# Performance work log

Hardware: AMD Instinct MI355X
Metric: run time of the kernel (lower is better)

Reference implementation:

```python
import jax, jax.numpy as jnp
import numpy as np

B, S, H = 2, 1024, 2048
NH, NKV, HD = 32, 8, 64
EPS = 1e-6
ROPE_BASE = 10000.0


def rms_norm(x, w, eps=EPS):
    xf = x.astype(jnp.float32)
    var = jnp.mean(xf * xf, axis=-1, keepdims=True)
    return (w * (xf * jax.lax.rsqrt(var + eps))).astype(x.dtype)


def rotate_half(x):
    x1, x2 = jnp.split(x, 2, axis=-1)
    return jnp.concatenate((-x2, x1), axis=-1)


def setup_inputs() -> dict:
    key = jax.random.key(0)
    ks = jax.random.split(key, 8)
    hidden_states = jax.random.normal(ks[0], (B, S, H), dtype=jnp.float32) * 0.02
    # real rotary embeddings for positions 0..S-1
    inv_freq = 1.0 / (ROPE_BASE ** (jnp.arange(0, HD, 2, dtype=jnp.float32) / HD))
    freqs = jnp.arange(S, dtype=jnp.float32)[:, None] * inv_freq[None, :]  # [S, HD/2]
    emb = jnp.concatenate((freqs, freqs), axis=-1)  # [S, HD]
    cos = jnp.broadcast_to(jnp.cos(emb)[None], (B, S, HD)).astype(jnp.float32)
    sin = jnp.broadcast_to(jnp.sin(emb)[None], (B, S, HD)).astype(jnp.float32)
    # additive causal mask [B, 1, S, S]
    causal = jnp.tril(jnp.ones((S, S), dtype=bool))
    attention_mask = jnp.broadcast_to(
        jnp.where(causal, 0.0, -1e9).astype(jnp.float32)[None, None], (B, 1, S, S))
    scale_in = 1.0 / np.sqrt(H)
    wq = jax.random.normal(ks[1], (H, NH * HD), dtype=jnp.float32) * scale_in
    wk = jax.random.normal(ks[2], (H, NKV * HD), dtype=jnp.float32) * scale_in
    wv = jax.random.normal(ks[3], (H, NKV * HD), dtype=jnp.float32) * scale_in
    wo = jax.random.normal(ks[4], (NH * HD, H), dtype=jnp.float32) * scale_in
    q_norm_w = jnp.ones((NH * HD,), dtype=jnp.float32)
    k_norm_w = jnp.ones((NKV * HD,), dtype=jnp.float32)
    return {"hidden_states": hidden_states, "cos": cos, "sin": sin,
            "attention_mask": attention_mask, "wq": wq, "wk": wk, "wv": wv,
            "wo": wo, "q_norm_w": q_norm_w, "k_norm_w": k_norm_w}


def reference(hidden_states, cos, sin, attention_mask, wq, wk, wv, wo, q_norm_w, k_norm_w):
    b, s, _ = hidden_states.shape
    scaling = HD ** -0.5
    groups = NH // NKV
    # projections + QK-norm (RMSNorm over full projected dim, before head split)
    q = rms_norm(hidden_states @ wq, q_norm_w)
    k = rms_norm(hidden_states @ wk, k_norm_w)
    v = hidden_states @ wv
    q = q.reshape(b, s, NH, HD).transpose(0, 2, 1, 3)   # [b, nh, s, hd]
    k = k.reshape(b, s, NKV, HD).transpose(0, 2, 1, 3)  # [b, nkv, s, hd]
    v = v.reshape(b, s, NKV, HD).transpose(0, 2, 1, 3)
    # RoPE (cos/sin broadcast over head dim)
    c = cos[:, None]  # [b, 1, s, hd]
    sn = sin[:, None]
    q = q * c + rotate_half(q) * sn
    k = k * c + rotate_half(k) * sn
    # GQA: repeat KV heads
    k = jnp.repeat(k, groups, axis=1)  # [b, nh, s, hd]
    v = jnp.repeat(v, groups, axis=1)
    scores = jnp.einsum('bhqd,bhkd->bhqk', q, k) * scaling + attention_mask
    attn = jax.nn.softmax(scores.astype(jnp.float32), axis=-1).astype(q.dtype)
    out = jnp.einsum('bhqk,bhkd->bhqd', attn, v)
    out = out.transpose(0, 2, 1, 3).reshape(b, s, NH * HD)
    return out @ wo
```

## Files before the change

kernel.cpp:

```cpp
#include <hip/hip_runtime.h>

#define B_    2
#define S_    1024
#define NH_   32
#define NKV_  8
#define T_    (B_*S_)

typedef unsigned short u16;
typedef unsigned int u32;
typedef __attribute__((ext_vector_type(8))) short bf16x8;
typedef __attribute__((ext_vector_type(4))) float f32x4;

__device__ __forceinline__ float bf2f(u16 u) {
    union { float f; unsigned int i; } c; c.i = ((unsigned int)u) << 16; return c.f;
}
__device__ __forceinline__ u32 cvtpk(float lo, float hi) {
    u32 r;
    asm("v_cvt_pk_bf16_f32 %0, %1, %2" : "=v"(r) : "v"(lo), "v"(hi));
    return r;
}
__device__ __forceinline__ u16 f2bf(float f) {
    return (u16)cvtpk(f, 0.f);
}

__device__ __forceinline__ void gld_lds16(const void* g, void* s) {
    __builtin_amdgcn_global_load_lds(
        (const __attribute__((address_space(1))) void*)g,
        (__attribute__((address_space(3))) void*)s,
        16, 0, 0);
}

__global__ __launch_bounds__(256) void preproc1(
    const float* __restrict__ hidden, const float* __restrict__ wq,
    const float* __restrict__ wk, const float* __restrict__ wv,
    const float* __restrict__ wo,
    u16* __restrict__ hidden_bf, u16* __restrict__ wqkvT, u16* __restrict__ woT)
{
    __shared__ float t[64][65];
    const int bid = blockIdx.x, tid = threadIdx.x;
    if (bid < 2048) {
        int i = (bid * 256 + tid) * 8;
        float4 v0 = *reinterpret_cast<const float4*>(&hidden[i]);
        float4 v1 = *reinterpret_cast<const float4*>(&hidden[i + 4]);
        u32 ow[4] = { cvtpk(v0.x, v0.y), cvtpk(v0.z, v0.w),
                      cvtpk(v1.x, v1.y), cvtpk(v1.z, v1.w) };
        *reinterpret_cast<uint4*>(&hidden_bf[i]) = *reinterpret_cast<uint4*>(ow);
        return;
    }
    const float* src; int scol, sN, n0, k0;
    u16* dst; int dK;
    if (bid < 3584) {
        const int tt = bid - 2048;
        n0 = (tt % 48) * 64; k0 = (tt / 48) * 64;
        if (n0 < 2048)      { src = wq; scol = n0;        sN = 2048; }
        else if (n0 < 2560) { src = wk; scol = n0 - 2048; sN = 512;  }
        else                { src = wv; scol = n0 - 2560; sN = 512;  }
        dst = wqkvT; dK = 2048;
    } else {
        const int tt = bid - 3584;
        n0 = (tt % 32) * 64; k0 = (tt / 32) * 64;
        src = wo; scol = n0; sN = 2048;
        dst = woT; dK = 2048;
    }
    #pragma unroll
    for (int i = 0; i < 4; ++i) {
        int e = i * 256 + tid, r = e >> 4, c4 = (e & 15) * 4;
        float4 v = *reinterpret_cast<const float4*>(
            &src[(size_t)(k0 + r) * sN + scol + c4]);
        t[r][c4 + 0] = v.x;
        t[r][c4 + 1] = v.y;
        t[r][c4 + 2] = v.z;
        t[r][c4 + 3] = v.w;
    }
    __syncthreads();
    #pragma unroll
    for (int i = 0; i < 4; ++i) {
        int e = i * 256 + tid, rr = e >> 4, cc4 = (e & 15) * 4;
        u32 ow[2] = { cvtpk(t[cc4][rr], t[cc4 + 1][rr]),
                      cvtpk(t[cc4 + 2][rr], t[cc4 + 3][rr]) };
        *reinterpret_cast<uint2*>(&dst[(size_t)(n0 + rr) * dK + k0 + cc4])
            = *reinterpret_cast<uint2*>(ow);
    }
}

template<int BM, int BN, bool OUT_BF16>
__global__ __launch_bounds__(256) void gemm_bt(
    const u16* __restrict__ A, const u16* __restrict__ Bt,
    void* __restrict__ Cv, int M, int N, int K)
{
    constexpr int FM  = BM / 32;
    constexpr int FN  = BN / 32;
    constexpr int ACH = BM / 32;
    constexpr int BCH = BN / 32;
    __shared__ u16 As[2][BM * 64];
    __shared__ u16 Bs[2][BN * 64];
    const int MB = M / BM;
    const int mpx = MB >> 3;
    const int xcd = blockIdx.x & 7, lid = blockIdx.x >> 3;
    const int bm = (xcd * mpx + (lid % mpx)) * BM;
    const int bn = (lid / mpx) * BN;
    const int tid = threadIdx.x;
    const int w = tid >> 6, lane = tid & 63;
    const int wr = w >> 1, wc = w & 1;
    const int l15 = lane & 15, lg = lane >> 4;
    const int srow = lane >> 3;
    const int scolsw = (lane & 7) ^ srow;

    f32x4 acc[FM][FN] = {};
    const int nk = K >> 6;

#define GSTAGE(ks, bb) do {                                                    \
    const int kofs = (ks) * 64;                                                \
    _Pragma("unroll")                                                          \
    for (int i_ = 0; i_ < ACH; ++i_) {                                         \
        int chunk_ = w * ACH + i_;                                             \
        int row_ = chunk_ * 8 + srow;                                          \
        gld_lds16(&A[(size_t)(bm + row_) * K + kofs + scolsw * 8],             \
                  &As[bb][chunk_ * 512]);                                      \
    }                                                                          \
    _Pragma("unroll")                                                          \
    for (int j_ = 0; j_ < BCH; ++j_) {                                         \
        int chunk_ = w * BCH + j_;                                             \
        int row_ = chunk_ * 8 + srow;                                          \
        gld_lds16(&Bt[(size_t)(bn + row_) * K + kofs + scolsw * 8],            \
                  &Bs[bb][chunk_ * 512]);                                      \
    } } while (0)

    GSTAGE(0, 0);
    for (int ks = 0; ks < nk; ++ks) {
        const int cur = ks & 1;
        if (ks + 1 < nk) {
            GSTAGE(ks + 1, cur ^ 1);
            if (ACH + BCH == 6)      { asm volatile("s_waitcnt vmcnt(6)" ::: "memory"); }
            else if (ACH + BCH == 4) { asm volatile("s_waitcnt vmcnt(4)" ::: "memory"); }
            else                     { asm volatile("s_waitcnt vmcnt(0)" ::: "memory"); }
        } else {
            asm volatile("s_waitcnt vmcnt(0)" ::: "memory");
        }
        __builtin_amdgcn_s_barrier();
        __builtin_amdgcn_sched_barrier(0);

        #pragma unroll
        for (int kk = 0; kk < 2; ++kk) {
            const int phys = ((kk * 4 + lg) ^ (l15 & 7)) * 8;
            bf16x8 a[FM], b[FN];
            #pragma unroll
            for (int m = 0; m < FM; ++m)
                a[m] = *reinterpret_cast<const bf16x8*>(
                    &As[cur][(wr * (BM / 2) + m * 16 + l15) * 64 + phys]);
            #pragma unroll
            for (int n = 0; n < FN; ++n)
                b[n] = *reinterpret_cast<const bf16x8*>(
                    &Bs[cur][(wc * (BN / 2) + n * 16 + l15) * 64 + phys]);
            #pragma unroll
            for (int m = 0; m < FM; ++m)
                #pragma unroll
                for (int n = 0; n < FN; ++n)
                    acc[m][n] = __builtin_amdgcn_mfma_f32_16x16x32_bf16(
                        a[m], b[n], acc[m][n], 0, 0, 0);
        }
        __builtin_amdgcn_s_barrier();
    }
#undef GSTAGE

    const int orow0 = bm + wr * (BM / 2), ocol0 = bn + wc * (BN / 2);
    #pragma unroll
    for (int m = 0; m < FM; ++m)
        #pragma unroll
        for (int n = 0; n < FN; ++n)
            #pragma unroll
            for (int r = 0; r < 4; ++r) {
                int row = orow0 + m * 16 + lg * 4 + r;
                int col = ocol0 + n * 16 + l15;
                float v = acc[m][n][r];
                if (OUT_BF16)
                    ((u16*)Cv)[(size_t)row * N + col] = f2bf(v);
                else
                    ((float*)Cv)[(size_t)row * N + col] = v;
            }
}

template<int DIM>
__device__ __forceinline__ void rms_rope_row(
    u16* base, const float* __restrict__ w,
    const float* __restrict__ cs, const float* __restrict__ sn,
    float* row, float* red, int tid, float osc)
{
    float ss = 0.f;
    for (int i0 = tid * 8; i0 < DIM; i0 += 2048) {
        uint4 u = *reinterpret_cast<const uint4*>(&base[i0]);
        const u16* us = reinterpret_cast<const u16*>(&u);
        #pragma unroll
        for (int j = 0; j < 8; ++j) { float f = bf2f(us[j]); row[i0 + j] = f; ss += f * f; }
    }
    #pragma unroll
    for (int off = 1; off < 64; off <<= 1) ss += __shfl_xor(ss, off);
    if ((tid & 63) == 0) red[tid >> 6] = ss;
    __syncthreads();
    const float rstd = rsqrtf((red[0] + red[1] + red[2] + red[3]) * (1.0f / DIM) + 1e-6f);

    for (int i0 = tid * 8; i0 < DIM; i0 += 2048) {
        float ov[8];
        #pragma unroll
        for (int j = 0; j < 8; ++j) {
            int i = i0 + j, dh = i & 63, bb = i & ~63;
            int oi = (dh < 32) ? bb + dh + 32 : bb + dh - 32;
            float y     = row[i]  * rstd * w[i];
            float other = row[oi] * rstd * w[oi];
            if (dh < 32) other = -other;
            ov[j] = (y * cs[dh] + other * sn[dh]) * osc;
        }
        u32 ow[4] = { cvtpk(ov[0], ov[1]), cvtpk(ov[2], ov[3]),
                      cvtpk(ov[4], ov[5]), cvtpk(ov[6], ov[7]) };
        *reinterpret_cast<uint4*>(&base[i0]) = *reinterpret_cast<uint4*>(ow);
    }
}

__global__ __launch_bounds__(256) void rmsnorm_rope_vt(
    u16* __restrict__ x, const float* __restrict__ qnw, const float* __restrict__ knw,
    const float* __restrict__ cosb, const float* __restrict__ sinb,
    u16* __restrict__ vT)
{
    __shared__ float smem[2304];
    const int bid = blockIdx.x, tid = threadIdx.x;
    if (bid < 2048) {
        const int t = bid;
        float* row = smem;
        float* red = smem + 2048;
        const float* cs = cosb + (size_t)t * 64;
        const float* sn = sinb + (size_t)t * 64;
        rms_rope_row<2048>(x + (size_t)t * 3072,        qnw, cs, sn, row, red, tid,
                           0.18033688f);
        __syncthreads();
        rms_rope_row<512 >(x + (size_t)t * 3072 + 2048, knw, cs, sn, row, red, tid,
                           1.0f);
        return;
    }
    u16 (*tu)[72] = reinterpret_cast<u16(*)[72]>(smem);
    const int bid2 = bid - 2048;
    const int hd = bid2 % 16;
    const int s0 = (bid2 / 16) * 64;
    const int b = hd >> 3, kvh = hd & 7;
    #pragma unroll
    for (int i = 0; i < 2; ++i) {
        int chunk = i * 256 + tid;
        int r = chunk >> 3, c8 = (chunk & 7) * 8;
        uint4 u = *reinterpret_cast<const uint4*>(
            &x[(size_t)(b * 1024 + s0 + r) * 3072 + 2560 + kvh * 64 + c8]);
        *reinterpret_cast<uint4*>(&tu[r][c8]) = u;
    }
    __syncthreads();
    #pragma unroll
    for (int i = 0; i < 2; ++i) {
        int chunk = i * 256 + tid;
        int d = chunk >> 3, c8 = (chunk & 7) * 8;
        u16 o[8];
        #pragma unroll
        for (int j = 0; j < 8; ++j) o[j] = tu[c8 + j][d];
        *reinterpret_cast<uint4*>(&vT[((size_t)(hd * 64 + d)) * 1024 + s0 + c8])
            = *reinterpret_cast<uint4*>(o);
    }
}

__global__ __launch_bounds__(256) void attn_tb(
    const u16* __restrict__ qkv,
    const u16* __restrict__ vT,
    u16* __restrict__ ob)
{
    __shared__ u16 Ks[3][64 * 64];
    __shared__ u16 Vs[3][64 * 64];
    __shared__ u16 Ps[4][16 * 64];

    const int bid = blockIdx.x;
    const int L   = (bid & 7) * 64 + (bid >> 3);
    const int g5  = L >> 5;
    const int rem = L & 31;
    const int ha  = rem & 3;
    const int p   = rem >> 2;
    const int b = g5 >> 3, kvh = g5 & 7;
    const int h = kvh * 4 + ha;
    const int qtA = p, qtB = 15 - p;

    const int tid = threadIdx.x, w = tid >> 6, lane = tid & 63;
    const int l15 = lane & 15, lg = lane >> 4;
    const int srow = lane >> 3;
    const int scolsw = (lane & 7) ^ srow;

    bf16x8 qfA[2], qfB[2];
    {
        const size_t rA = (size_t)(b * 1024 + qtA * 64 + w * 16 + l15);
        const size_t rB = (size_t)(b * 1024 + qtB * 64 + w * 16 + l15);
        #pragma unroll
        for (int kk = 0; kk < 2; ++kk) {
            qfA[kk] = *reinterpret_cast<const bf16x8*>(
                &qkv[rA * 3072 + h * 64 + kk * 32 + lg * 8]);
            qfB[kk] = *reinterpret_cast<const bf16x8*>(
                &qkv[rB * 3072 + h * 64 + kk * 32 + lg * 8]);
        }
    }
    asm volatile("s_waitcnt vmcnt(0)" ::: "memory");

    float lrA = 0.f, lrB = 0.f;
    f32x4 oaccA[4] = {}, oaccB[4] = {};

    const u16* kbase = qkv + 2048 + kvh * 64;
    const u16* vbase = vT + (size_t)(g5 * 64) * 1024;
    const int qgA = qtA * 64 + w * 16 + l15;
    const int qgB = qtB * 64 + w * 16 + l15;

#define ASTAGE(kt, bb) do {                                                    \
    _Pragma("unroll")                                                          \
    for (int i_ = 0; i_ < 2; ++i_) {                                           \
        int chunk_ = w * 2 + i_;                                               \
        int row_ = chunk_ * 8 + srow;                                          \
        gld_lds16(&kbase[(size_t)(b * 1024 + (kt) * 64 + row_) * 3072          \
                         + scolsw * 8], &Ks[bb][chunk_ * 512]);                \
        gld_lds16(&vbase[(size_t)row_ * 1024 + (kt) * 64 + scolsw * 8],        \
                  &Vs[bb][chunk_ * 512]);                                      \
    } } while (0)

    auto step = [&](int kt, int cur, const bf16x8 (&qf)[2],
                    float& lr, f32x4 (&oacc)[4], int qg, bool dz) {
        f32x4 sacc[4] = {};
        #pragma unroll
        for (int kk = 0; kk < 2; ++kk) {
            const int phys = ((kk * 4 + lg) ^ (l15 & 7)) * 8;
            #pragma unroll
            for (int m = 0; m < 4; ++m) {
                bf16x8 kf = *reinterpret_cast<const bf16x8*>(
                    &Ks[cur][(m * 16 + l15) * 64 + phys]);
                sacc[m] = __builtin_amdgcn_mfma_f32_16x16x32_bf16(
                    kf, qf[kk], sacc[m], 0, 0, 0);
            }
        }

        float pv[4][4];
        if (dz) {
            #pragma unroll
            for (int m = 0; m < 4; ++m)
                #pragma unroll
                for (int r = 0; r < 4; ++r) {
                    float v = sacc[m][r];
                    if (kt * 64 + m * 16 + lg * 4 + r > qg) v = -1e30f;
                    pv[m][r] = exp2f(v);
                }
        } else {
            #pragma unroll
            for (int m = 0; m < 4; ++m)
                #pragma unroll
                for (int r = 0; r < 4; ++r)
                    pv[m][r] = exp2f(sacc[m][r]);
        }
        float ls = 0.f;
        #pragma unroll
        for (int m = 0; m < 4; ++m) {
            ls += (pv[m][0] + pv[m][1]) + (pv[m][2] + pv[m][3]);
            u32 pkw[2] = { cvtpk(pv[m][0], pv[m][1]),
                           cvtpk(pv[m][2], pv[m][3]) };
            const int keyc = m * 16 + lg * 4;
            const int phys = (keyc >> 3) ^ (l15 & 7);
            *reinterpret_cast<uint2*>(&Ps[w][l15 * 64 + phys * 8 + (keyc & 7)])
                = *reinterpret_cast<const uint2*>(pkw);
        }
        lr += ls;

        #pragma unroll
        for (int kk = 0; kk < 2; ++kk) {
            const int phys = ((kk * 4 + lg) ^ (l15 & 7)) * 8;
            bf16x8 pf = *reinterpret_cast<const bf16x8*>(
                &Ps[w][l15 * 64 + phys]);
            #pragma unroll
            for (int d = 0; d < 4; ++d) {
                bf16x8 vf = *reinterpret_cast<const bf16x8*>(
                    &Vs[cur][(d * 16 + l15) * 64 + phys]);
                oacc[d] = __builtin_amdgcn_mfma_f32_16x16x32_bf16(
                    pf, vf, oacc[d], 0, 0, 0);
            }
        }
    };

    ASTAGE(0, 0);
    for (int s = 0; s <= 16; ++s) {
        const int cur = s % 3;
        if (s < 16) {
            const int ktn = (s + 1 <= p) ? (s + 1) : (s - p);
            ASTAGE(ktn, (s + 1) % 3);
            asm volatile("s_waitcnt vmcnt(4)" ::: "memory");
        } else {
            asm volatile("s_waitcnt vmcnt(0)" ::: "memory");
        }
        __builtin_amdgcn_s_barrier();
        __builtin_amdgcn_sched_barrier(0);

        if (s <= p) step(s,         cur, qfA, lrA, oaccA, qgA, s == p);
        else        step(s - p - 1, cur, qfB, lrB, oaccB, qgB, s == 16);
    }
#undef ASTAGE

    #pragma unroll
    for (int tt = 0; tt < 2; ++tt) {
        const int qt = tt ? qtB : qtA;
        float lsum = tt ? lrB : lrA;
        lsum += __shfl_xor(lsum, 16);
        lsum += __shfl_xor(lsum, 32);
        f32x4* oacc = tt ? oaccB : oaccA;
        float linv[4];
        #pragma unroll
        for (int r = 0; r < 4; ++r) {
            float lv = __shfl(lsum, (lane & 48) + ((lane >> 4) & 3) * 4 + r);
            linv[r] = 1.f / lv;
        }
        #pragma unroll
        for (int d = 0; d < 4; ++d)
            #pragma unroll
            for (int r = 0; r < 4; ++r)
                ob[(size_t)(b * 1024 + qt * 64 + w * 16 + lg * 4 + r) * 2048
                   + h * 64 + d * 16 + l15] = f2bf(oacc[d][r] * linv[r]);
    }
}

extern "C" void kernel_launch(void* const* d_in, const int* in_sizes, int n_in,
                              void* d_out, int out_size, void* d_ws, size_t ws_size,
                              hipStream_t stream)
{
    const float* hidden = (const float*)d_in[0];
    const float* cosb   = (const float*)d_in[1];
    const float* sinb   = (const float*)d_in[2];
    const float* wq     = (const float*)d_in[4];
    const float* wk     = (const float*)d_in[5];
    const float* wv     = (const float*)d_in[6];
    const float* wo     = (const float*)d_in[7];
    const float* qnw    = (const float*)d_in[8];
    const float* knw    = (const float*)d_in[9];
    float* out = (float*)d_out;

    char* ws = (char*)d_ws;
    u16* hidden_bf = (u16*)ws;
    u16* wqkvT     = (u16*)(ws + ((size_t)8  << 20));
    u16* attn_bf   = (u16*)(ws + ((size_t)8  << 20));
    u16* qkv_bf    = (u16*)(ws + ((size_t)20 << 20));
    u16* v_bfT     = (u16*)(ws + ((size_t)32 << 20));
    u16* woT       = (u16*)(ws + ((size_t)34 << 20));

    preproc1<<<4608, 256, 0, stream>>>(hidden, wq, wk, wv, wo,
                                       hidden_bf, wqkvT, woT);

    gemm_bt<128, 64, true><<<768, 256, 0, stream>>>(hidden_bf, wqkvT, qkv_bf,
                                                    2048, 3072, 2048);

    rmsnorm_rope_vt<<<2304, 256, 0, stream>>>(qkv_bf, qnw, knw, cosb, sinb, v_bfT);

    attn_tb<<<512, 256, 0, stream>>>(qkv_bf, v_bfT, attn_bf);

    gemm_bt<64, 64, false><<<1024, 256, 0, stream>>>(attn_bf, woT, out,
                                                     2048, 2048, 2048);
}
```

Baseline: 116.6 us.

## Split attention into 32-row paired strips with 2-wave blocks and double buffering

Rewrites the causal attention kernel to use 128-thread blocks that each process two 32-row query strips (p and 31-p), launching 1024 blocks instead of 512. K/V staging drops from triple to double buffering, with an extra barrier per step to protect buffer reuse. The aim is finer work granularity and better load balance and occupancy across CUs. In exchange, each K/V tile load serves only half as many query rows, and the extra barrier reduces overlap between loads and compute.

```diff
diff --git a/kernel.cpp b/kernel.cpp
--- a/kernel.cpp
+++ b/kernel.cpp
@@ -262,24 +262,25 @@
     }
 }
 
-__global__ __launch_bounds__(256) void attn_tb(
+__global__ __launch_bounds__(128) void attn_pair(
     const u16* __restrict__ qkv,
     const u16* __restrict__ vT,
     u16* __restrict__ ob)
 {
-    __shared__ u16 Ks[3][64 * 64];
-    __shared__ u16 Vs[3][64 * 64];
-    __shared__ u16 Ps[4][16 * 64];
+    __shared__ u16 Ks[2][64 * 64];
+    __shared__ u16 Vs[2][64 * 64];
+    __shared__ u16 Ps[2][16 * 64];
 
     const int bid = blockIdx.x;
-    const int L   = (bid & 7) * 64 + (bid >> 3);
-    const int g5  = L >> 5;
-    const int rem = L & 31;
+    const int L   = (bid & 7) * 128 + (bid >> 3);
+    const int g5  = L >> 6;
+    const int rem = L & 63;
     const int ha  = rem & 3;
     const int p   = rem >> 2;
     const int b = g5 >> 3, kvh = g5 & 7;
     const int h = kvh * 4 + ha;
-    const int qtA = p, qtB = 15 - p;
+    const int spA = p, spB = 31 - p;
+    const int tilesA = (p >> 1) + 1;
 
     const int tid = threadIdx.x, w = tid >> 6, lane = tid & 63;
     const int l15 = lane & 15, lg = lane >> 4;
@@ -288,8 +289,8 @@
 
     bf16x8 qfA[2], qfB[2];
     {
-        const size_t rA = (size_t)(b * 1024 + qtA * 64 + w * 16 + l15);
-        const size_t rB = (size_t)(b * 1024 + qtB * 64 + w * 16 + l15);
+        const size_t rA = (size_t)(b * 1024 + spA * 32 + w * 16 + l15);
+        const size_t rB = (size_t)(b * 1024 + spB * 32 + w * 16 + l15);
         #pragma unroll
         for (int kk = 0; kk < 2; ++kk) {
             qfA[kk] = *reinterpret_cast<const bf16x8*>(
@@ -305,13 +306,13 @@
 
     const u16* kbase = qkv + 2048 + kvh * 64;
     const u16* vbase = vT + (size_t)(g5 * 64) * 1024;
-    const int qgA = qtA * 64 + w * 16 + l15;
-    const int qgB = qtB * 64 + w * 16 + l15;
+    const int qgA = spA * 32 + w * 16 + l15;
+    const int qgB = spB * 32 + w * 16 + l15;
 
 #define ASTAGE(kt, bb) do {                                                    \
     _Pragma("unroll")                                                          \
-    for (int i_ = 0; i_ < 2; ++i_) {                                           \
-        int chunk_ = w * 2 + i_;                                               \
+    for (int i_ = 0; i_ < 4; ++i_) {                                           \
+        int chunk_ = w * 4 + i_;                                               \
         int row_ = chunk_ * 8 + srow;                                          \
         gld_lds16(&kbase[(size_t)(b * 1024 + (kt) * 64 + row_) * 3072          \
                          + scolsw * 8], &Ks[bb][chunk_ * 512]);                \
@@ -381,25 +382,30 @@
 
     ASTAGE(0, 0);
     for (int s = 0; s <= 16; ++s) {
-        const int cur = s % 3;
+        const int cur = s & 1;
         if (s < 16) {
-            const int ktn = (s + 1 <= p) ? (s + 1) : (s - p);
-            ASTAGE(ktn, (s + 1) % 3);
-            asm volatile("s_waitcnt vmcnt(4)" ::: "memory");
+            const int sn = s + 1;
+            const int ktn = (sn < tilesA) ? sn : (sn - tilesA);
+            ASTAGE(ktn, cur ^ 1);
+            asm volatile("s_waitcnt vmcnt(8)" ::: "memory");
         } else {
             asm volatile("s_waitcnt vmcnt(0)" ::: "memory");
         }
         __builtin_amdgcn_s_barrier();
         __builtin_amdgcn_sched_barrier(0);
 
-        if (s <= p) step(s,         cur, qfA, lrA, oaccA, qgA, s == p);
-        else        step(s - p - 1, cur, qfB, lrB, oaccB, qgB, s == 16);
+        if (s < tilesA)
+            step(s,          cur, qfA, lrA, oaccA, qgA, s == tilesA - 1);
+        else
+            step(s - tilesA, cur, qfB, lrB, oaccB, qgB, s == 16);
+
+        __builtin_amdgcn_s_barrier();
     }
 #undef ASTAGE
 
     #pragma unroll
     for (int tt = 0; tt < 2; ++tt) {
-        const int qt = tt ? qtB : qtA;
+        const int sp = tt ? spB : spA;
         float lsum = tt ? lrB : lrA;
         lsum += __shfl_xor(lsum, 16);
         lsum += __shfl_xor(lsum, 32);
@@ -414,7 +420,7 @@
         for (int d = 0; d < 4; ++d)
             #pragma unroll
             for (int r = 0; r < 4; ++r)
-                ob[(size_t)(b * 1024 + qt * 64 + w * 16 + lg * 4 + r) * 2048
+                ob[(size_t)(b * 1024 + sp * 32 + w * 16 + lg * 4 + r) * 2048
                    + h * 64 + d * 16 + l15] = f2bf(oacc[d][r] * linv[r]);
     }
 }
@@ -450,7 +456,7 @@
 
     rmsnorm_rope_vt<<<2304, 256, 0, stream>>>(qkv_bf, qnw, knw, cosb, sinb, v_bfT);
 
-    attn_tb<<<512, 256, 0, stream>>>(qkv_bf, v_bfT, attn_bf);
+    attn_pair<<<1024, 128, 0, stream>>>(qkv_bf, v_bfT, attn_bf);
 
     gemm_bt<64, 64, false><<<1024, 256, 0, stream>>>(attn_bf, woT, out,
                                                      2048, 2048, 2048);
```

Measured after the change: 118.8 us. Within noise of the previous version (+1.9%).
